# Kernel tuning notes

Measured on AMD Instinct MI355X. Metric: run time of the kernel, lower is better.

The kernel has to match this reference:

```python
import jax, jax.numpy as jnp
import numpy as np

K = 24          # SiFinder.KERNEL_SIZE
SIGMA = 1e-6    # SiFinder.CORR_SIGMA


def setup_inputs() -> dict:
    key = jax.random.key(0)
    k1, k2, k3 = jax.random.split(key, 3)
    H = W = 480
    x_dec = jax.random.normal(k1, (1, 3, H, W), dtype=jnp.float32)
    y_dec = jax.random.normal(k2, (1, 3, H, W), dtype=jnp.float32)
    y = jax.random.normal(k3, (1, 3, H, W), dtype=jnp.float32)
    return {"x_dec": x_dec, "y_dec": y_dec, "y": y}


def _get_x_patches(x_dec):
    # non-overlapping KxK patches, raster order (rows of patches, then cols)
    _, C, H, W = x_dec.shape
    p = x_dec[0].reshape(C, H // K, K, W // K, K)
    return p.transpose(1, 3, 0, 2, 4).reshape(-1, C, K, K)  # (P, C, K, K)


def _conv(img, w):
    # valid cross-correlation, matches F.conv2d
    return jax.lax.conv_general_dilated(
        img, w, window_strides=(1, 1), padding='VALID',
        dimension_numbers=('NCHW', 'OIHW', 'NCHW'))


def _pearson_corr(x_patches, y):
    C = x_patches.shape[1]
    ps = C * K * K  # patch_size
    mean_x = jnp.mean(x_patches, axis=(1, 2, 3))[None, :, None, None]   # (1,P,1,1)
    sum_x2 = jnp.sum(x_patches ** 2, axis=(1, 2, 3))[None, :, None, None]
    ones = jnp.ones((1, C, K, K), y.dtype)
    sum_y = _conv(y, ones)            # (1,1,H',W'); torch builds P identical channels
    xy = _conv(y, x_patches)          # (1,P,H',W')
    numer = xy / ps - mean_x * sum_y / ps
    den_x = sum_x2 / ps - mean_x ** 2
    den_y = _conv(y ** 2, ones) / ps - sum_y ** 2 / ps ** 2
    return (2 * numer + SIGMA) / (jnp.abs(den_x) + jnp.abs(den_y) + SIGMA)


def _forward(x_dec, y_dec, y):
    x_patches = _get_x_patches(x_dec)
    corr = _pearson_corr(x_patches, y_dec)          # (1, P, H', W')
    _, P, Hc, Wc = corr.shape
    idx = jnp.argmax(corr[0].reshape(P, Hc * Wc), axis=-1)
    rows, cols = idx // Wc, idx % Wc
    # roi_align(boxes=[-0.5+c, -0.5+r, ...], out=KxK, sampling_ratio=-1) samples
    # exactly at integer pixel centers -> reduces to an exact patch gather from y.
    C = y.shape[1]
    def take(r, c):
        return jax.lax.dynamic_slice(y[0], (0, r, c), (C, K, K))
    patches = jax.vmap(take)(rows, cols)            # (P, C, K, K)
    # nn.Fold with stride==kernel: stitch non-overlapping patches back to image
    H, W = x_dec.shape[2], x_dec.shape[3]
    img = patches.reshape(H // K, W // K, C, K, K).transpose(2, 0, 3, 1, 4)
    return img.reshape(1, C, H, W)


def reference(x_dec, y_dec, y):
    return _forward(x_dec, y_dec, y)
```

## Files before the change

kernel.cpp:

```cpp
#include <hip/hip_runtime.h>
#include <stdint.h>

#define HW    480
#define KS    24
#define CH    3
#define HO    457
#define NPOS  (HO*HO)
#define NP    400
#define PS    (CH*KS*KS)
#define SIG   1e-6f
#define NSQ   54
#define NMT   14
#define NIY   115
#define NGRP  (NIY*8*4)
#define MAXF  16384
#define RGRID 4096
#define DELTA 4e-3f
#define QS    28.0f
#define IS2   (1.0f/(QS*QS))
#define PB    2608

typedef __attribute__((ext_vector_type(4)))  int  int4v;
typedef __attribute__((ext_vector_type(16))) int  int16v;
typedef unsigned int uint;
typedef unsigned char uchar;
typedef unsigned long long ull;

static __device__ __forceinline__ char q8(float v) {
    float s = rintf(v * QS);
    s = fminf(127.f, fmaxf(-127.f, s));
    return (char)(int)s;
}
static __device__ __forceinline__ uint mono(float f) {
    uint u = __float_as_uint(f);
    return (u & 0x80000000u) ? ~u : (u | 0x80000000u);
}
static __device__ __forceinline__ float unmono(uint u) {
    uint b = (u & 0x80000000u) ? (u & 0x7fffffffu) : ~u;
    return __uint_as_float(b);
}

__global__ void fat1_k(const float* __restrict__ x, const float* __restrict__ yd,
                       float* __restrict__ Wp, char* __restrict__ yq,
                       float* __restrict__ cs, float* __restrict__ cs2) {
    int b = blockIdx.x;
    if (b < 2700) {
        int t = b * 256 + threadIdx.x;
        int p = t / PS, e = t - p * PS;
        int c = e / (KS * KS);
        int r = (e / KS) % KS;
        int w = e % KS;
        int pr = p / 20, pc = p - pr * 20;
        Wp[t] = x[c * HW * HW + (pr * KS + r) * HW + (pc * KS + w)];
    } else if (b < 5400) {
        int t = (b - 2700) * 256 + threadIdx.x;
        yq[t] = q8(yd[t]);
    } else {
        int t = (b - 5400) * 256 + threadIdx.x;
        if (t >= HO * HW) return;
        int i = t / HW, w = t - i * HW;
        float s = 0.f, s2 = 0.f;
        for (int c = 0; c < CH; c++) {
            const float* base = yd + c * HW * HW + i * HW + w;
            for (int dh = 0; dh < KS; dh++) {
                float v = base[dh * HW];
                s += v; s2 += v * v;
            }
        }
        cs[t] = s; cs2[t] = s2;
    }
}

__global__ void fat2_k(const float* __restrict__ Wp,
                       const float* __restrict__ cs, const float* __restrict__ cs2,
                       float* __restrict__ meanX, float* __restrict__ denXa,
                       char* __restrict__ Aq,
                       float* __restrict__ sumY, float* __restrict__ denYa,
                       uint* __restrict__ cnt, ull* __restrict__ best) {
    __shared__ float shs[4], shs2[4];
    int b = blockIdx.x;
    if (b < 400) {
        int p = b;
        if (threadIdx.x == 1) best[p] = 0ull;
        if (b == 0 && threadIdx.x == 2) *cnt = 0u;
        float s = 0.f, s2 = 0.f;
        for (int e = threadIdx.x; e < PS; e += 256) {
            float v = Wp[p * PS + e];
            s += v; s2 += v * v;
        }
        for (int o = 32; o > 0; o >>= 1) { s += __shfl_down(s, o); s2 += __shfl_down(s2, o); }
        int lane = threadIdx.x & 63, wv = threadIdx.x >> 6;
        if (lane == 0) { shs[wv] = s; shs2[wv] = s2; }
        __syncthreads();
        if (threadIdx.x == 0) {
            float S = shs[0] + shs[1] + shs[2] + shs[3];
            float S2 = shs2[0] + shs2[1] + shs2[2] + shs2[3];
            float m = S / (float)PS;
            meanX[p] = m;
            denXa[p] = fabsf(S2 / (float)PS - m * m);
        }
    } else if (b < 3424) {
        int id = (b - 400) * 256 + threadIdx.x;
        int e    = id & 15;
        int lane = (id >> 4) & 63;
        int f    = id >> 10;
        int s    = f % NSQ;
        int mtg  = f / NSQ;
        int kk = s * 32 + (lane >> 5) * 16 + e;
        int p  = mtg * 32 + (lane & 31);
        float v = (p < NP) ? Wp[p * PS + kk] : 0.f;
        Aq[id] = q8(v);
    } else {
        int t = (b - 3424) * 256 + threadIdx.x;
        if (t >= NPOS) return;
        int i = t / HO, j = t - i * HO;
        const float* r  = cs  + i * HW + j;
        const float* r2 = cs2 + i * HW + j;
        float s = 0.f, s2 = 0.f;
        for (int d = 0; d < KS; d++) { s += r[d]; s2 += r2[d]; }
        sumY[t] = s;
        float ips = 1.0f / (float)PS;
        denYa[t] = fabsf(s2 * ips - (s * ips) * (s * ips));
    }
}

__launch_bounds__(256, 3)
__global__ void corr1_k(const char* __restrict__ yq, const char* __restrict__ Aq,
                        const float* __restrict__ meanX, const float* __restrict__ denXa,
                        const float* __restrict__ sumY, const float* __restrict__ denYa,
                        uint* __restrict__ table) {
    __shared__ __align__(16) uchar S[8 * PB];

    const int tid  = threadIdx.x;
    const int lane = tid & 63;
    const int g    = tid >> 6;
    const int n    = lane & 31;
    const int kha  = lane >> 5;
    const int jx   = blockIdx.x;
    const int iy   = blockIdx.y;
    const int mtp  = blockIdx.z;
    const int j0   = 64 * jx;
    const int i0   = 4 * iy;
    const int i    = i0 + g;

    const int olo0 = kha ? 16  : 0,   ohi0 = kha ? 96  : 8;
    const int olo1 = kha ? 192 : 104, ohi1 = kha ? 200 : 112;
    const int olo2 = kha ? 296 : 208, ohi2 = kha ? 304 : 288;

    const uchar* Bt0g = S + ((2 * n) & 7) * PB + ((2 * n) & ~7) + g * 96;
    const uchar* Bt1g = Bt0g + PB;

    const char* A0 = Aq + ((size_t)(mtp * 2 + 0) * NSQ << 10) + lane * 16;
    const char* A1 = Aq + ((size_t)(mtp * 2 + 1) * NSQ << 10) + lane * 16;

    int16v acc[2][2];
#pragma unroll
    for (int mt = 0; mt < 2; mt++)
#pragma unroll
        for (int t = 0; t < 2; t++) acc[mt][t] = (int16v)0;

    for (int c = 0; c < CH; c++) {
        __syncthreads();
        for (int it = tid; it < 27 * 6; it += 256) {
            int row = it / 6;
            int gb  = (it - row * 6) * 16;
            int yr  = i0 + row;
            int gj  = j0 + gb;
            uint d[6];
            if (yr < HW && gj + 24 <= HW) {
                const uchar* src = (const uchar*)yq + ((size_t)(c * HW + yr)) * HW + gj;
                uint4 a = *(const uint4*)src;
                uint2 bb = *(const uint2*)(src + 16);
                d[0] = a.x; d[1] = a.y; d[2] = a.z; d[3] = a.w; d[4] = bb.x; d[5] = bb.y;
            } else {
                uchar tmp[24];
#pragma unroll
                for (int e = 0; e < 24; e++) {
                    int col = gj + e;
                    tmp[e] = (yr < HW && col < HW)
                           ? ((const uchar*)yq)[((size_t)(c * HW + yr)) * HW + col] : (uchar)0;
                }
                const uint* tp = (const uint*)tmp;
#pragma unroll
                for (int e = 0; e < 6; e++) d[e] = tp[e];
            }
            int base = row * 96 + gb;
#pragma unroll
            for (int pi = 0; pi < 8; pi++) {
                const int a = pi >> 2;
                const int r = pi & 3;
                uint4 w;
                if (r == 0)
                    w = make_uint4(d[a], d[a + 1], d[a + 2], d[a + 3]);
                else
                    w = make_uint4((d[a]     >> (8 * r)) | (d[a + 1] << (32 - 8 * r)),
                                   (d[a + 1] >> (8 * r)) | (d[a + 2] << (32 - 8 * r)),
                                   (d[a + 2] >> (8 * r)) | (d[a + 3] << (32 - 8 * r)),
                                   (d[a + 3] >> (8 * r)) | (d[a + 4] << (32 - 8 * r)));
                *(uint4*)&S[pi * PB + base] = w;
            }
        }
        __syncthreads();

        const char* A0c = A0 + ((size_t)(c * 18) << 10);
        const char* A1c = A1 + ((size_t)(c * 18) << 10);
        for (int q = 0; q < 6; q++) {
            const char* A0q = A0c + ((size_t)(3 * q) << 10);
            const char* A1q = A1c + ((size_t)(3 * q) << 10);
            int4v a0v[3], a1v[3];
#pragma unroll
            for (int u = 0; u < 3; u++) {
                a0v[u] = *(const int4v*)(A0q + (u << 10));
                a1v[u] = *(const int4v*)(A1q + (u << 10));
            }
            const uchar* Bq0 = Bt0g + 384 * q;
            const uchar* Bq1 = Bt1g + 384 * q;
#pragma unroll
            for (int u = 0; u < 3; u++) {
                const int olo = (u == 0) ? olo0 : (u == 1) ? olo1 : olo2;
                const int ohi = (u == 0) ? ohi0 : (u == 1) ? ohi1 : ohi2;
#pragma unroll
                for (int t = 0; t < 2; t++) {
                    const uchar* Bq = t ? Bq1 : Bq0;
                    uint2 lo = *(const uint2*)(Bq + olo);
                    uint2 hi = *(const uint2*)(Bq + ohi);
                    int4v bv;
                    bv.x = (int)lo.x; bv.y = (int)lo.y; bv.z = (int)hi.x; bv.w = (int)hi.y;
                    acc[0][t] = __builtin_amdgcn_mfma_i32_32x32x32_i8(a0v[u], bv, acc[0][t], 0, 0, 0);
                    acc[1][t] = __builtin_amdgcn_mfma_i32_32x32x32_i8(a1v[u], bv, acc[1][t], 0, 0, 0);
                }
            }
        }
    }

    const int grp = (iy * 8 + jx) * 4 + g;
    const float c2 = 2.0f / (float)PS;
    const bool iok = i < HO;
    float sYv[2], rDv[2];
#pragma unroll
    for (int t = 0; t < 2; t++) {
        int j = j0 + 2 * n + t;
        bool ok = iok && (j < HO);
        sYv[t] = ok ? sumY[i * HO + j] : 0.f;
        rDv[t] = ok ? denYa[i * HO + j] : 0.f;
    }
    const bool jv0 = iok && (j0 + 2 * n + 0 < HO);
    const bool jv1 = iok && (j0 + 2 * n + 1 < HO);
#pragma unroll
    for (int mt = 0; mt < 2; mt++) {
        const int pbase = (mtp * 2 + mt) * 32;
#pragma unroll
        for (int r = 0; r < 16; r++) {
            int p = pbase + (r & 3) + 8 * (r >> 2) + 4 * kha;
            bool pok = p < NP;
            float mX = pok ? meanX[p] : 0.f;
            float dX = pok ? denXa[p] : 0.f;
            float bu = -3.0e38f;
#pragma unroll
            for (int t = 0; t < 2; t++) {
                bool ok = t ? jv1 : jv0;
                if (ok) {
                    float xy = (float)acc[mt][t][r] * IS2;
                    float numer = fmaf(-mX, sYv[t], xy) * c2 + SIG;
                    float rp = __builtin_amdgcn_rcpf(dX + rDv[t] + SIG);
                    bu = fmaxf(bu, numer * rp);
                }
            }
#pragma unroll
            for (int o = 1; o < 32; o <<= 1)
                bu = fmaxf(bu, __shfl_xor(bu, o));
            if (n == 0 && pok) table[p * NGRP + grp] = mono(bu);
        }
    }
}

__global__ void flag_k(const uint* __restrict__ table,
                       uint* __restrict__ flags, uint* __restrict__ cnt) {
    __shared__ uint sm[4];
    __shared__ float sthr;
    int p = blockIdx.x;
    uint m = 0;
    for (int g = threadIdx.x; g < NGRP; g += 256) {
        uint v = table[p * NGRP + g];
        m = v > m ? v : m;
    }
    for (int o = 32; o > 0; o >>= 1) { uint ot = __shfl_down(m, o); m = ot > m ? ot : m; }
    int lane = threadIdx.x & 63, wv = threadIdx.x >> 6;
    if (lane == 0) sm[wv] = m;
    __syncthreads();
    if (threadIdx.x == 0) {
        uint mm = max(max(sm[0], sm[1]), max(sm[2], sm[3]));
        sthr = unmono(mm) - DELTA;
    }
    __syncthreads();
    float thr = sthr;
    for (int g = threadIdx.x; g < NGRP; g += 256) {
        if (unmono(table[p * NGRP + g]) >= thr) {
            uint idx = atomicAdd(cnt, 1u);
            if (idx < MAXF) flags[idx] = (uint)(p * NGRP + g);
        }
    }
}

__launch_bounds__(64)
__global__ void rescore_k(const float* __restrict__ Wp, const float* __restrict__ y_dec,
                          const float* __restrict__ meanX, const float* __restrict__ denXa,
                          const float* __restrict__ sumY, const float* __restrict__ denYa,
                          const uint* __restrict__ flags, const uint* __restrict__ cnt,
                          ull* __restrict__ best) {
    uint nflag = *cnt; if (nflag > MAXF) nflag = MAXF;
    for (uint fb = blockIdx.x; fb < nflag; fb += RGRID) {
        uint f = flags[fb];
        int p = f / NGRP, grp = f - p * NGRP;
        int g = grp & 3, bj = grp >> 2;
        int jx = bj & 7, iy = bj >> 3;
        int i = 4 * iy + g;
        int j = 64 * jx + threadIdx.x;
        ull pk = 0;
        if (i < HO && j < HO) {
            float dot = 0.f;
            const float* wr = Wp + p * PS;
            for (int c = 0; c < CH; c++)
                for (int kh = 0; kh < KS; kh++) {
                    const float* yr = y_dec + ((c * HW) + i + kh) * HW + j;
                    const float* wk = wr + (c * KS + kh) * KS;
#pragma unroll
                    for (int kw = 0; kw < KS; kw++) dot += wk[kw] * yr[kw];
                }
            float corr = (2.0f * (dot - meanX[p] * sumY[i * HO + j]) * (1.0f / (float)PS) + SIG)
                       / (denXa[p] + denYa[i * HO + j] + SIG);
            uint idx = (uint)(i * HO + j);
            pk = ((ull)mono(corr) << 32) | (uint)(~idx);
        }
        for (int o = 32; o > 0; o >>= 1) { ull ot = __shfl_down(pk, o); pk = ot > pk ? ot : pk; }
        if (threadIdx.x == 0) atomicMax(&best[p], pk);
    }
}

__global__ void gather_k(const float* __restrict__ y,
                         const ull* __restrict__ best,
                         float* __restrict__ out) {
    int p = blockIdx.x;
    uint idx = ~((uint)(best[p] & 0xFFFFFFFFull));
    int r = idx / HO, cc = idx - r * HO;
    int pr = p / 20, pc = p - pr * 20;
    for (int e = threadIdx.x; e < PS; e += 256) {
        int c = e / (KS * KS);
        int kh = (e / KS) % KS;
        int kw = e % KS;
        out[c * HW * HW + (pr * KS + kh) * HW + (pc * KS + kw)] =
            y[c * HW * HW + (r + kh) * HW + (cc + kw)];
    }
}

extern "C" void kernel_launch(void* const* d_in, const int* in_sizes, int n_in,
                              void* d_out, int out_size, void* d_ws, size_t ws_size,
                              hipStream_t stream) {
    const float* x_dec = (const float*)d_in[0];
    const float* y_dec = (const float*)d_in[1];
    const float* y     = (const float*)d_in[2];
    float* out = (float*)d_out;

    char* ws = (char*)d_ws;
    size_t off = 0;
    auto carve = [&](size_t bytes) -> void* {
        void* p = ws + off;
        off += (bytes + 255) & ~(size_t)255;
        return p;
    };
    float*  Wp    = (float*)carve((size_t)NP * PS * 4);
    char*   yq    = (char*)carve((size_t)CH * HW * HW);
    char*   Aq    = (char*)carve((size_t)NMT * NSQ * 1024);
    float*  cs    = (float*)carve((size_t)HO * HW * 4);
    float*  cs2   = (float*)carve((size_t)HO * HW * 4);
    float*  sumY  = (float*)carve((size_t)NPOS * 4);
    float*  denYa = (float*)carve((size_t)NPOS * 4);
    float*  meanX = (float*)carve((size_t)NP * 4);
    float*  denXa = (float*)carve((size_t)NP * 4);
    uint*   table = (uint*)carve((size_t)NP * NGRP * 4);
    uint*   flags = (uint*)carve((size_t)MAXF * 4);
    uint*   cnt   = (uint*)carve(256);
    ull*    best  = (ull*)carve((size_t)NP * 8);

    fat1_k<<<6257, 256, 0, stream>>>(x_dec, y_dec, Wp, yq, cs, cs2);
    fat2_k<<<4240, 256, 0, stream>>>(Wp, cs, cs2, meanX, denXa, Aq, sumY, denYa, cnt, best);

    dim3 grid(8, NIY, 7);
    corr1_k<<<grid, 256, 0, stream>>>(yq, Aq, meanX, denXa, sumY, denYa, table);

    flag_k<<<NP, 256, 0, stream>>>(table, flags, cnt);
    rescore_k<<<RGRID, 64, 0, stream>>>(Wp, y_dec, meanX, denXa, sumY, denYa, flags, cnt, best);

    gather_k<<<NP, 256, 0, stream>>>(y, best, out);
}
```

Before: 402.3 us.

## Fuse flag, rescore and gather into one per-patch kernel; restructure prep kernels

Merges the threshold-flag, exact rescoring and final patch gather into a single per-patch kernel that builds its flag list in shared memory, rescoring one candidate per wavefront. This removes the global atomic counter, the best-value atomics and two launches. The prep stage is reorganised so Aq, meanX and denXa are computed straight from x_dec inside the first kernel, leaving the second kernel only the window sums. The trade-off is that rescoring is now limited to one 256-thread block per patch, so a patch with many flagged candidates runs serially.

```diff
diff --git a/kernel.cpp b/kernel.cpp
--- a/kernel.cpp
+++ b/kernel.cpp
@@ -13,8 +13,6 @@
 #define NMT   14
 #define NIY   115
 #define NGRP  (NIY*8*4)
-#define MAXF  16384
-#define RGRID 4096
 #define DELTA 4e-3f
 #define QS    28.0f
 #define IS2   (1.0f/(QS*QS))
@@ -42,7 +40,10 @@
 
 __global__ void fat1_k(const float* __restrict__ x, const float* __restrict__ yd,
                        float* __restrict__ Wp, char* __restrict__ yq,
-                       float* __restrict__ cs, float* __restrict__ cs2) {
+                       float* __restrict__ cs, float* __restrict__ cs2,
+                       char* __restrict__ Aq,
+                       float* __restrict__ meanX, float* __restrict__ denXa) {
+    __shared__ float shs[4], shs2[4];
     int b = blockIdx.x;
     if (b < 2700) {
         int t = b * 256 + threadIdx.x;
@@ -55,7 +56,7 @@
     } else if (b < 5400) {
         int t = (b - 2700) * 256 + threadIdx.x;
         yq[t] = q8(yd[t]);
-    } else {
+    } else if (b < 6257) {
         int t = (b - 5400) * 256 + threadIdx.x;
         if (t >= HO * HW) return;
         int i = t / HW, w = t - i * HW;
@@ -68,39 +69,8 @@
             }
         }
         cs[t] = s; cs2[t] = s2;
-    }
-}
-
-__global__ void fat2_k(const float* __restrict__ Wp,
-                       const float* __restrict__ cs, const float* __restrict__ cs2,
-                       float* __restrict__ meanX, float* __restrict__ denXa,
-                       char* __restrict__ Aq,
-                       float* __restrict__ sumY, float* __restrict__ denYa,
-                       uint* __restrict__ cnt, ull* __restrict__ best) {
-    __shared__ float shs[4], shs2[4];
-    int b = blockIdx.x;
-    if (b < 400) {
-        int p = b;
-        if (threadIdx.x == 1) best[p] = 0ull;
-        if (b == 0 && threadIdx.x == 2) *cnt = 0u;
-        float s = 0.f, s2 = 0.f;
-        for (int e = threadIdx.x; e < PS; e += 256) {
-            float v = Wp[p * PS + e];
-            s += v; s2 += v * v;
-        }
-        for (int o = 32; o > 0; o >>= 1) { s += __shfl_down(s, o); s2 += __shfl_down(s2, o); }
-        int lane = threadIdx.x & 63, wv = threadIdx.x >> 6;
-        if (lane == 0) { shs[wv] = s; shs2[wv] = s2; }
-        __syncthreads();
-        if (threadIdx.x == 0) {
-            float S = shs[0] + shs[1] + shs[2] + shs[3];
-            float S2 = shs2[0] + shs2[1] + shs2[2] + shs2[3];
-            float m = S / (float)PS;
-            meanX[p] = m;
-            denXa[p] = fabsf(S2 / (float)PS - m * m);
-        }
-    } else if (b < 3424) {
-        int id = (b - 400) * 256 + threadIdx.x;
+    } else if (b < 9281) {
+        int id = (b - 6257) * 256 + threadIdx.x;
         int e    = id & 15;
         int lane = (id >> 4) & 63;
         int f    = id >> 10;
@@ -108,20 +78,52 @@
         int mtg  = f / NSQ;
         int kk = s * 32 + (lane >> 5) * 16 + e;
         int p  = mtg * 32 + (lane & 31);
-        float v = (p < NP) ? Wp[p * PS + kk] : 0.f;
+        float v = 0.f;
+        if (p < NP) {
+            int c  = kk / (KS * KS);
+            int r  = (kk / KS) % KS;
+            int w  = kk % KS;
+            int pr = p / 20, pc = p - pr * 20;
+            v = x[c * HW * HW + (pr * KS + r) * HW + (pc * KS + w)];
+        }
         Aq[id] = q8(v);
     } else {
-        int t = (b - 3424) * 256 + threadIdx.x;
-        if (t >= NPOS) return;
-        int i = t / HO, j = t - i * HO;
-        const float* r  = cs  + i * HW + j;
-        const float* r2 = cs2 + i * HW + j;
+        int p = b - 9281;
+        int pr = p / 20, pc = p - pr * 20;
         float s = 0.f, s2 = 0.f;
-        for (int d = 0; d < KS; d++) { s += r[d]; s2 += r2[d]; }
-        sumY[t] = s;
-        float ips = 1.0f / (float)PS;
-        denYa[t] = fabsf(s2 * ips - (s * ips) * (s * ips));
-    }
+        for (int e = threadIdx.x; e < PS; e += 256) {
+            int c = e / (KS * KS);
+            int r = (e / KS) % KS;
+            int w = e % KS;
+            float v = x[c * HW * HW + (pr * KS + r) * HW + (pc * KS + w)];
+            s += v; s2 += v * v;
+        }
+        for (int o = 32; o > 0; o >>= 1) { s += __shfl_down(s, o); s2 += __shfl_down(s2, o); }
+        int lane = threadIdx.x & 63, wv = threadIdx.x >> 6;
+        if (lane == 0) { shs[wv] = s; shs2[wv] = s2; }
+        __syncthreads();
+        if (threadIdx.x == 0) {
+            float S = shs[0] + shs[1] + shs[2] + shs[3];
+            float S2 = shs2[0] + shs2[1] + shs2[2] + shs2[3];
+            float m = S / (float)PS;
+            meanX[p] = m;
+            denXa[p] = fabsf(S2 / (float)PS - m * m);
+        }
+    }
+}
+
+__global__ void fat2_k(const float* __restrict__ cs, const float* __restrict__ cs2,
+                       float* __restrict__ sumY, float* __restrict__ denYa) {
+    int t = blockIdx.x * 256 + threadIdx.x;
+    if (t >= NPOS) return;
+    int i = t / HO, j = t - i * HO;
+    const float* r  = cs  + i * HW + j;
+    const float* r2 = cs2 + i * HW + j;
+    float s = 0.f, s2 = 0.f;
+    for (int d = 0; d < KS; d++) { s += r[d]; s2 += r2[d]; }
+    sumY[t] = s;
+    float ips = 1.0f / (float)PS;
+    denYa[t] = fabsf(s2 * ips - (s * ips) * (s * ips));
 }
 
 __launch_bounds__(256, 3)
@@ -274,77 +276,85 @@
     }
 }
 
-__global__ void flag_k(const uint* __restrict__ table,
-                       uint* __restrict__ flags, uint* __restrict__ cnt) {
+__global__ void final_k(const uint* __restrict__ table,
+                        const float* __restrict__ Wp, const float* __restrict__ y_dec,
+                        const float* __restrict__ meanX, const float* __restrict__ denXa,
+                        const float* __restrict__ sumY, const float* __restrict__ denYa,
+                        const float* __restrict__ y, float* __restrict__ out) {
     __shared__ uint sm[4];
     __shared__ float sthr;
-    int p = blockIdx.x;
+    __shared__ uint fl[2048];
+    __shared__ uint scnt;
+    __shared__ ull sb4[4];
+
+    const int p = blockIdx.x;
+    const int tid = threadIdx.x;
+    const int ln = tid & 63, wv = tid >> 6;
+    const uint* trow = table + (size_t)p * NGRP;
+
     uint m = 0;
-    for (int g = threadIdx.x; g < NGRP; g += 256) {
-        uint v = table[p * NGRP + g];
+    for (int g = tid; g < NGRP; g += 256) {
+        uint v = trow[g];
         m = v > m ? v : m;
     }
     for (int o = 32; o > 0; o >>= 1) { uint ot = __shfl_down(m, o); m = ot > m ? ot : m; }
-    int lane = threadIdx.x & 63, wv = threadIdx.x >> 6;
-    if (lane == 0) sm[wv] = m;
+    if (ln == 0) sm[wv] = m;
     __syncthreads();
-    if (threadIdx.x == 0) {
+    if (tid == 0) {
         uint mm = max(max(sm[0], sm[1]), max(sm[2], sm[3]));
         sthr = unmono(mm) - DELTA;
     }
     __syncthreads();
-    float thr = sthr;
-    for (int g = threadIdx.x; g < NGRP; g += 256) {
-        if (unmono(table[p * NGRP + g]) >= thr) {
-            uint idx = atomicAdd(cnt, 1u);
-            if (idx < MAXF) flags[idx] = (uint)(p * NGRP + g);
-        }
-    }
-}
-
-__launch_bounds__(64)
-__global__ void rescore_k(const float* __restrict__ Wp, const float* __restrict__ y_dec,
-                          const float* __restrict__ meanX, const float* __restrict__ denXa,
-                          const float* __restrict__ sumY, const float* __restrict__ denYa,
-                          const uint* __restrict__ flags, const uint* __restrict__ cnt,
-                          ull* __restrict__ best) {
-    uint nflag = *cnt; if (nflag > MAXF) nflag = MAXF;
-    for (uint fb = blockIdx.x; fb < nflag; fb += RGRID) {
-        uint f = flags[fb];
-        int p = f / NGRP, grp = f - p * NGRP;
-        int g = grp & 3, bj = grp >> 2;
-        int jx = bj & 7, iy = bj >> 3;
-        int i = 4 * iy + g;
-        int j = 64 * jx + threadIdx.x;
-        ull pk = 0;
-        if (i < HO && j < HO) {
-            float dot = 0.f;
-            const float* wr = Wp + p * PS;
-            for (int c = 0; c < CH; c++)
-                for (int kh = 0; kh < KS; kh++) {
-                    const float* yr = y_dec + ((c * HW) + i + kh) * HW + j;
-                    const float* wk = wr + (c * KS + kh) * KS;
-#pragma unroll
-                    for (int kw = 0; kw < KS; kw++) dot += wk[kw] * yr[kw];
-                }
-            float corr = (2.0f * (dot - meanX[p] * sumY[i * HO + j]) * (1.0f / (float)PS) + SIG)
-                       / (denXa[p] + denYa[i * HO + j] + SIG);
-            uint idx = (uint)(i * HO + j);
-            pk = ((ull)mono(corr) << 32) | (uint)(~idx);
-        }
-        for (int o = 32; o > 0; o >>= 1) { ull ot = __shfl_down(pk, o); pk = ot > pk ? ot : pk; }
-        if (threadIdx.x == 0) atomicMax(&best[p], pk);
-    }
-}
-
-__global__ void gather_k(const float* __restrict__ y,
-                         const ull* __restrict__ best,
-                         float* __restrict__ out) {
-    int p = blockIdx.x;
-    uint idx = ~((uint)(best[p] & 0xFFFFFFFFull));
+    const float thr = sthr;
+
+    ull wbest = 0;
+    const float* wr = Wp + (size_t)p * PS;
+    const float mX = meanX[p], dX = denXa[p];
+    for (int cs0 = 0; cs0 < NGRP; cs0 += 2048) {
+        if (tid == 0) scnt = 0;
+        __syncthreads();
+        int cend = cs0 + 2048 < NGRP ? cs0 + 2048 : NGRP;
+        for (int g = cs0 + tid; g < cend; g += 256) {
+            if (unmono(trow[g]) >= thr) fl[atomicAdd(&scnt, 1u)] = (uint)g;
+        }
+        __syncthreads();
+        uint nf = scnt;
+        for (uint fi = wv; fi < nf; fi += 4) {
+            uint grp = fl[fi];
+            int gq = grp & 3, bj = grp >> 2;
+            int jx = bj & 7, iy = bj >> 3;
+            int i = 4 * iy + gq;
+            int j = 64 * jx + ln;
+            ull pk = 0;
+            if (i < HO && j < HO) {
+                float dot = 0.f;
+                for (int c = 0; c < CH; c++)
+                    for (int kh = 0; kh < KS; kh++) {
+                        const float* yr = y_dec + ((c * HW) + i + kh) * HW + j;
+                        const float* wk = wr + (c * KS + kh) * KS;
+#pragma unroll
+                        for (int kw = 0; kw < KS; kw++) dot += wk[kw] * yr[kw];
+                    }
+                float corr = (2.0f * (dot - mX * sumY[i * HO + j]) * (1.0f / (float)PS) + SIG)
+                           / (dX + denYa[i * HO + j] + SIG);
+                uint idx = (uint)(i * HO + j);
+                pk = ((ull)mono(corr) << 32) | (uint)(~idx);
+            }
+            for (int o = 32; o > 0; o >>= 1) { ull ot = __shfl_down(pk, o); pk = ot > pk ? ot : pk; }
+            if (ln == 0) wbest = pk > wbest ? pk : wbest;
+        }
+        __syncthreads();
+    }
+    if (ln == 0) sb4[wv] = wbest;
+    __syncthreads();
+
+    ull b0 = sb4[0] > sb4[1] ? sb4[0] : sb4[1];
+    ull b1 = sb4[2] > sb4[3] ? sb4[2] : sb4[3];
+    ull bb = b0 > b1 ? b0 : b1;
+    uint idx = ~((uint)(bb & 0xFFFFFFFFull));
     int r = idx / HO, cc = idx - r * HO;
     int pr = p / 20, pc = p - pr * 20;
-    for (int e = threadIdx.x; e < PS; e += 256) {
+    for (int e = tid; e < PS; e += 256) {
         int c = e / (KS * KS);
         int kh = (e / KS) % KS;
         int kw = e % KS;
@@ -378,18 +388,12 @@
     float*  meanX = (float*)carve((size_t)NP * 4);
     float*  denXa = (float*)carve((size_t)NP * 4);
     uint*   table = (uint*)carve((size_t)NP * NGRP * 4);
-    uint*   flags = (uint*)carve((size_t)MAXF * 4);
-    uint*   cnt   = (uint*)carve(256);
-    ull*    best  = (ull*)carve((size_t)NP * 8);
-
-    fat1_k<<<6257, 256, 0, stream>>>(x_dec, y_dec, Wp, yq, cs, cs2);
-    fat2_k<<<4240, 256, 0, stream>>>(Wp, cs, cs2, meanX, denXa, Aq, sumY, denYa, cnt, best);
+
+    fat1_k<<<9681, 256, 0, stream>>>(x_dec, y_dec, Wp, yq, cs, cs2, Aq, meanX, denXa);
+    fat2_k<<<816, 256, 0, stream>>>(cs, cs2, sumY, denYa);
 
     dim3 grid(8, NIY, 7);
     corr1_k<<<grid, 256, 0, stream>>>(yq, Aq, meanX, denXa, sumY, denYa, table);
 
-    flag_k<<<NP, 256, 0, stream>>>(table, flags, cnt);
-    rescore_k<<<RGRID, 64, 0, stream>>>(Wp, y_dec, meanX, denXa, sumY, denYa, flags, cnt, best);
-
-    gather_k<<<NP, 256, 0, stream>>>(y, best, out);
-}
+    final_k<<<NP, 256, 0, stream>>>(table, Wp, y_dec, meanX, denXa, sumY, denYa, y, out);
+}
```

Measured after the change: 441.4 us. 9.7% more time.
